# Kernel tuning notes

Measured on AMD Instinct MI355X. Metric: run time of the kernel, lower is better.

Reference implementation:

```python
import jax, jax.numpy as jnp
import numpy as np

N = 50000   # total nodes in batch
E = 640000  # directed edges
G = 64      # graphs in batch
D_IN = 128
D_H = 128
D_OUT = 10


def _glorot(key, shape):
    fan_in = shape[0]
    return jax.random.normal(key, shape, dtype=jnp.float32) / np.sqrt(fan_in)


def setup_inputs() -> dict:
    key = jax.random.key(0)
    ks = jax.random.split(key, 10)
    x = jax.random.normal(ks[0], (N, D_IN), dtype=jnp.float32)
    src = jax.random.randint(ks[1], (E,), 0, N, dtype=jnp.int32)
    dst = jax.random.randint(ks[2], (E,), 0, N, dtype=jnp.int32)
    batch = jnp.sort(jax.random.randint(ks[3], (N,), 0, G, dtype=jnp.int32))
    return {
        "x": x, "src": src, "dst": dst, "batch": batch,
        "W1": _glorot(ks[4], (D_IN, D_H)), "b1": jnp.zeros((D_H,), jnp.float32),
        "W2": _glorot(ks[5], (D_H, D_H)), "b2": jnp.zeros((D_H,), jnp.float32),
        "W3": _glorot(ks[6], (D_H, D_H)), "b3": jnp.zeros((D_H,), jnp.float32),
        "Wl": _glorot(ks[7], (D_H, D_OUT)), "bl": jnp.zeros((D_OUT,), jnp.float32),
    }


def gcn_conv(x, W, b, src, dst):
    """PyG GCNConv: add self-loops, symmetric deg^-1/2 normalization,
    linear transform, scatter-sum aggregation at dst, plus bias."""
    n = x.shape[0]
    loops = jnp.arange(n, dtype=src.dtype)
    s = jnp.concatenate([src, loops])  # [E+N]
    d = jnp.concatenate([dst, loops])
    deg = jax.ops.segment_sum(jnp.ones_like(d, dtype=x.dtype), d, num_segments=n)
    dinv = jnp.where(deg > 0, jax.lax.rsqrt(deg), 0.0)
    norm = dinv[s] * dinv[d]                        # [E+N]
    h = x @ W                                       # [N, D]
    out = jax.ops.segment_sum(h[s] * norm[:, None], d, num_segments=n)
    return out + b


def reference(x, src, dst, batch, W1, b1, W2, b2, W3, b3, Wl, bl):
    n = x.shape[0]
    h = jax.nn.relu(gcn_conv(x, W1, b1, src, dst))
    # dropout is a no-op in eval mode
    h = jax.nn.relu(gcn_conv(h, W2, b2, src, dst))
    h = gcn_conv(h, W3, b3, src, dst)
    # global_mean_pool over graph ids
    sums = jax.ops.segment_sum(h, batch, num_segments=G)            # [G, D]
    counts = jax.ops.segment_sum(jnp.ones((n,), h.dtype), batch, num_segments=G)
    pooled = sums / jnp.maximum(counts, 1.0)[:, None]
    logits = pooled @ Wl + bl                                       # [G, D_OUT]
    return jax.nn.log_softmax(logits, axis=1)
```

## Files before the change

### kernel.cpp

```cpp
#include <hip/hip_runtime.h>


constexpr int D = 128;
constexpr int DOUT = 10;
constexpr int PSPLIT = 8;
constexpr int BSH = 3;
constexpr int BCAP = 192;
constexpr int CPAD = 16;

using short8  = __attribute__((ext_vector_type(8))) short;
using float4v = __attribute__((ext_vector_type(4))) float;
using f32x2   = __attribute__((ext_vector_type(2))) float;

__device__ __forceinline__ ushort f2bf(float f) {
  uint u = __float_as_uint(f);
  return (ushort)((u + 0x7fffu + ((u >> 16) & 1u)) >> 16);
}
__device__ __forceinline__ float bf2f(ushort s) {
  return __uint_as_float(((uint)s) << 16);
}
__device__ __forceinline__ float bfhi(uint u) { return __uint_as_float(u & 0xffff0000u); }


__global__ void init_kernel(int* __restrict__ bcnt, int total) {
  int i = blockIdx.x * blockDim.x + threadIdx.x;
  if (i < total) bcnt[i] = 0;
}

__global__ void binfill_kernel(const int* __restrict__ src, const int* __restrict__ dst,
    int* __restrict__ bcnt, uint* __restrict__ buck, int e) {
  int i = blockIdx.x * blockDim.x + threadIdx.x;
  if (i >= e) return;
  int d = dst[i], s = src[i];
  int b = d >> BSH;
  int pos = atomicAdd(&bcnt[b * CPAD], 1);
  if (pos < BCAP)
    buck[(size_t)b * BCAP + pos] = (uint)s | ((uint)(d & ((1 << BSH) - 1)) << 16);
}

__global__ __launch_bounds__(256) void countb_kernel(const uint* __restrict__ buck,
    const int* __restrict__ bcnt, int* __restrict__ cnt, float* __restrict__ dinv,
    int* __restrict__ bsum, int n) {
  __shared__ int lc[256];
  const int base = blockIdx.x * 256;
  const int m = min(256, n - base);
  lc[threadIdx.x] = 0;
  __syncthreads();
  const int b0 = base >> BSH;
  #pragma unroll
  for (int bb = 0; bb < (256 >> BSH); ++bb) {
    int b = b0 + bb;
    if ((b << BSH) >= n) break;
    int c = min(bcnt[b * CPAD], BCAP);
    for (int i = threadIdx.x; i < c; i += 256)
      atomicAdd(&lc[(bb << BSH) + (int)(buck[(size_t)b * BCAP + i] >> 16)], 1);
  }
  __syncthreads();
  int v = lc[threadIdx.x];
  if ((int)threadIdx.x < m) {
    cnt[base + threadIdx.x] = v;
    dinv[base + threadIdx.x] = rsqrtf((float)(v + 1));
  }
  __shared__ int sd[256];
  sd[threadIdx.x] = ((int)threadIdx.x < m) ? v : 0;
  __syncthreads();
  for (int off = 128; off > 0; off >>= 1) {
    if (threadIdx.x < (unsigned)off) sd[threadIdx.x] += sd[threadIdx.x + off];
    __syncthreads();
  }
  if (threadIdx.x == 0) bsum[blockIdx.x] = sd[0];
}

__global__ __launch_bounds__(1024) void scan2_kernel(const int* __restrict__ bsum,
    int* __restrict__ boff, int nb, int* __restrict__ rowptr, int n) {
  __shared__ int sd[1024];
  int v = ((int)threadIdx.x < nb) ? bsum[threadIdx.x] : 0;
  sd[threadIdx.x] = v;
  __syncthreads();
  for (int off = 1; off < 1024; off <<= 1) {
    int t = (threadIdx.x >= (unsigned)off) ? sd[threadIdx.x - off] : 0;
    __syncthreads();
    sd[threadIdx.x] += t;
    __syncthreads();
  }
  if ((int)threadIdx.x < nb) boff[threadIdx.x] = sd[threadIdx.x] - v;
  if ((int)threadIdx.x == nb - 1) rowptr[n] = sd[threadIdx.x];
}

__global__ __launch_bounds__(256) void scatter_kernel(const uint* __restrict__ buck,
    const int* __restrict__ bcnt, const int* __restrict__ cnt,
    const int* __restrict__ boff, int* __restrict__ rowptr,
    const float* __restrict__ dinv, uint* __restrict__ epk, int n) {
  __shared__ int sd[256];
  __shared__ int lcur[256];
  const int base = blockIdx.x * 256;
  const int i = base + (int)threadIdx.x;
  int v = (i < n) ? cnt[i] : 0;
  sd[threadIdx.x] = v;
  __syncthreads();
  for (int off = 1; off < 256; off <<= 1) {
    int t = (threadIdx.x >= (unsigned)off) ? sd[threadIdx.x - off] : 0;
    __syncthreads();
    sd[threadIdx.x] += t;
    __syncthreads();
  }
  int rp = boff[blockIdx.x] + sd[threadIdx.x] - v;
  if (i < n) {
    rowptr[i] = rp;
    lcur[threadIdx.x] = rp;
  }
  __syncthreads();
  const int b0 = base >> BSH;
  #pragma unroll
  for (int bb = 0; bb < (256 >> BSH); ++bb) {
    int b = b0 + bb;
    if ((b << BSH) >= n) break;
    int c = min(bcnt[b * CPAD], BCAP);
    for (int j = threadIdx.x; j < c; j += 256) {
      uint rec = buck[(size_t)b * BCAP + j];
      int dl = (int)(rec >> 16);
      int s = (int)(rec & 0xffffu);
      int d = (b << BSH) + dl;
      int slot = atomicAdd(&lcur[(bb << BSH) + dl], 1);
      epk[slot] = (uint)s | ((uint)f2bf(dinv[s] * dinv[d]) << 16);
    }
  }
}

__global__ __launch_bounds__(256) void prepw_kernel(const float* __restrict__ W1,
    const float* __restrict__ W2, const float* __restrict__ W3, ushort* __restrict__ Wp) {
  const float* W = (blockIdx.y == 0) ? W1 : (blockIdx.y == 1) ? W2 : W3;
  ushort* Wpo = Wp + (size_t)blockIdx.y * 2048 * 8;
  int idx = blockIdx.x * 256 + threadIdx.x;
  int cf = idx >> 8, kk = (idx >> 6) & 3, lane = idx & 63;
  int k0 = kk * 32 + (lane >> 4) * 8;
  int c = cf * 16 + (lane & 15);
  uint p[4];
  #pragma unroll
  for (int h = 0; h < 4; ++h) {
    ushort lo = f2bf(W[(k0 + 2 * h) * D + c]);
    ushort hi = f2bf(W[(k0 + 2 * h + 1) * D + c]);
    p[h] = (uint)lo | ((uint)hi << 16);
  }
  uint4 w = make_uint4(p[0], p[1], p[2], p[3]);
  *(uint4*)(Wpo + idx * 8) = w;
}

__global__ __launch_bounds__(256) void gemm_mfma(const float* __restrict__ Ain,
    const ushort* __restrict__ Wp, uchar* __restrict__ out, int n) {
  __shared__ ushort wl[2048 * 8];
  const int tid = threadIdx.x;
  #pragma unroll
  for (int i = 0; i < 8; ++i) {
    int idx = tid + i * 256;
    *(uint4*)(&wl[idx * 8]) = *(const uint4*)(Wp + idx * 8);
  }
  __syncthreads();
  const int w = tid >> 6, lane = tid & 63;
  const int row0 = blockIdx.x * 64 + w * 16;
  int arow = row0 + (lane & 15);
  if (arow >= n) arow = n - 1;

  short8 a[4];
  const float* abase = Ain + (size_t)arow * D + ((lane >> 4) * 8);
  #pragma unroll
  for (int kk = 0; kk < 4; ++kk) {
    float4 f0 = *(const float4*)(abase + kk * 32);
    float4 f1 = *(const float4*)(abase + kk * 32 + 4);
    short8 v;
    v[0] = (short)f2bf(f0.x); v[1] = (short)f2bf(f0.y);
    v[2] = (short)f2bf(f0.z); v[3] = (short)f2bf(f0.w);
    v[4] = (short)f2bf(f1.x); v[5] = (short)f2bf(f1.y);
    v[6] = (short)f2bf(f1.z); v[7] = (short)f2bf(f1.w);
    a[kk] = v;
  }

  float4v acc[8] = {};
  #pragma unroll
  for (int kk = 0; kk < 4; ++kk) {
    #pragma unroll
    for (int cf = 0; cf < 8; ++cf) {
      short8 b = *(const short8*)(&wl[((cf * 4 + kk) * 64 + lane) * 8]);
      acc[cf] = __builtin_amdgcn_mfma_f32_16x16x32_bf16(a[kk], b, acc[cf], 0, 0, 0);
    }
  }
  const int crow = row0 + (lane >> 4) * 4;
  const int ccol = lane & 15;
  #pragma unroll
  for (int cf = 0; cf < 8; ++cf) {
    #pragma unroll
    for (int r = 0; r < 4; ++r) {
      if (crow + r < n) {
        int enc = __builtin_amdgcn_cvt_pk_fp8_f32(acc[cf][r], acc[cf][r], 0, false);
        out[(size_t)(crow + r) * D + cf * 16 + ccol] = (uchar)(enc & 0xff);
      }
    }
  }
}

__device__ __forceinline__ void agg_node(const uchar* __restrict__ h8,
    const int* __restrict__ rowptr, const uint* __restrict__ epk,
    const float* __restrict__ dinv, const float* __restrict__ bias,
    int node, int sub, int li, int relu,
    float& a0, float& a1, float& a2, float& a3) {
  const int beg = rowptr[node], end = rowptr[node + 1];
  a0 = a1 = a2 = a3 = 0.f;
  for (int e = beg; e < end; e += 16) {
    uint mm[8], rr[8];
    #pragma unroll
    for (int k = 0; k < 8; ++k)
      mm[k] = epk[min(e + 2 * k + sub, end - 1)];
    #pragma unroll
    for (int k = 0; k < 8; ++k)
      rr[k] = *(const uint*)(h8 + (size_t)(mm[k] & 0xffffu) * D + li * 4);
    #pragma unroll
    for (int k = 0; k < 8; ++k) {
      float wk = (e + 2 * k + sub < end) ? bfhi(mm[k]) : 0.f;
      f32x2 pa = __builtin_amdgcn_cvt_pk_f32_fp8(rr[k], false);
      f32x2 pb = __builtin_amdgcn_cvt_pk_f32_fp8(rr[k], true);
      a0 += pa[0] * wk;
      a1 += pa[1] * wk;
      a2 += pb[0] * wk;
      a3 += pb[1] * wk;
    }
  }
  a0 += __shfl_xor(a0, 32);
  a1 += __shfl_xor(a1, 32);
  a2 += __shfl_xor(a2, 32);
  a3 += __shfl_xor(a3, 32);
  const float di = dinv[node];
  const float dsq = di * di;
  uint sv = *(const uint*)(h8 + (size_t)node * D + li * 4);
  f32x2 sa = __builtin_amdgcn_cvt_pk_f32_fp8(sv, false);
  f32x2 sb = __builtin_amdgcn_cvt_pk_f32_fp8(sv, true);
  a0 += sa[0] * dsq;
  a1 += sa[1] * dsq;
  a2 += sb[0] * dsq;
  a3 += sb[1] * dsq;
  float4 bv = *(const float4*)(bias + li * 4);
  a0 += bv.x; a1 += bv.y; a2 += bv.z; a3 += bv.w;
  if (relu) {
    a0 = fmaxf(a0, 0.f); a1 = fmaxf(a1, 0.f);
    a2 = fmaxf(a2, 0.f); a3 = fmaxf(a3, 0.f);
  }
}

__global__ __launch_bounds__(256) void aggemm_kernel(const uchar* __restrict__ h8,
    const int* __restrict__ rowptr, const uint* __restrict__ epk,
    const float* __restrict__ dinv, const float* __restrict__ bias,
    const ushort* __restrict__ Wp, uchar* __restrict__ out8, int n) {
  __shared__ ushort At[16][136];
  const int wv = (int)(threadIdx.x >> 6);
  const int lane = (int)(threadIdx.x & 63);
  const int sub = lane >> 5;
  const int li = lane & 31;
  const int node0 = blockIdx.x * 16;
  #pragma unroll
  for (int t = 0; t < 4; ++t) {
    const int row = wv * 4 + t;
    const int node = node0 + row;
    if (node < n) {
      float a0, a1, a2, a3;
      agg_node(h8, rowptr, epk, dinv, bias, node, sub, li, 1, a0, a1, a2, a3);
      if (sub == 0) {
        uint2 pk;
        pk.x = (uint)f2bf(a0) | ((uint)f2bf(a1) << 16);
        pk.y = (uint)f2bf(a2) | ((uint)f2bf(a3) << 16);
        *(uint2*)(&At[row][li * 4]) = pk;
      }
    } else if (sub == 0) {
      *(uint2*)(&At[row][li * 4]) = make_uint2(0, 0);
    }
  }
  __syncthreads();
  const int r = lane & 15;
  const int koff = (lane >> 4) * 8;
  short8 a[4];
  #pragma unroll
  for (int kk = 0; kk < 4; ++kk)
    a[kk] = *(const short8*)(&At[r][koff + kk * 32]);
  const int crow = node0 + (lane >> 4) * 4;
  const int ccol = lane & 15;
  #pragma unroll
  for (int cc = 0; cc < 2; ++cc) {
    const int cf = wv * 2 + cc;
    float4v acc = {};
    #pragma unroll
    for (int kk = 0; kk < 4; ++kk) {
      short8 b = *(const short8*)(Wp + (size_t)((cf * 4 + kk) * 64 + lane) * 8);
      acc = __builtin_amdgcn_mfma_f32_16x16x32_bf16(a[kk], b, acc, 0, 0, 0);
    }
    #pragma unroll
    for (int r2 = 0; r2 < 4; ++r2) {
      if (crow + r2 < n) {
        int enc = __builtin_amdgcn_cvt_pk_fp8_f32(acc[r2], acc[r2], 0, false);
        out8[(size_t)(crow + r2) * D + cf * 16 + ccol] = (uchar)(enc & 0xff);
      }
    }
  }
}

__global__ __launch_bounds__(256) void agg_kernel(const uchar* __restrict__ h8,
    const int* __restrict__ rowptr, const uint* __restrict__ epk,
    const float* __restrict__ dinv, const float* __restrict__ bias,
    ushort* __restrict__ out, int n, int relu) {
  int node = (int)((blockIdx.x * blockDim.x + threadIdx.x) >> 6);
  if (node >= n) return;
  const int lane = threadIdx.x & 63;
  const int sub = lane >> 5;
  const int li = lane & 31;
  float a0, a1, a2, a3;
  agg_node(h8, rowptr, epk, dinv, bias, node, sub, li, relu, a0, a1, a2, a3);
  if (sub == 0) {
    uint2 pk;
    pk.x = (uint)f2bf(a0) | ((uint)f2bf(a1) << 16);
    pk.y = (uint)f2bf(a2) | ((uint)f2bf(a3) << 16);
    *(uint2*)(out + (size_t)node * D + li * 4) = pk;
  }
}

__global__ __launch_bounds__(256) void pool1_kernel(const ushort* __restrict__ act,
    const int* __restrict__ batch, float* __restrict__ pp, int n) {
  const int g = blockIdx.x;
  const int sp = blockIdx.y;
  int lo = 0, hi = n;
  while (lo < hi) { int mid = (lo + hi) >> 1; if (batch[mid] < g) lo = mid + 1; else hi = mid; }
  const int start = lo;
  hi = n;
  while (lo < hi) { int mid = (lo + hi) >> 1; if (batch[mid] <= g) lo = mid + 1; else hi = mid; }
  const int end = lo;
  const int len = end - start;
  const int per = (len + PSPLIT - 1) / PSPLIT;
  const int i0 = start + sp * per;
  const int i1 = min(i0 + per, end);

  const int rt = threadIdx.x >> 4;
  const int ds = threadIdx.x & 15;
  float acc[8] = {};
  for (int i = i0 + rt; i < i1; i += 16) {
    short8 v = *(const short8*)(act + (size_t)i * D + ds * 8);
    #pragma unroll
    for (int e2 = 0; e2 < 8; ++e2) acc[e2] += bf2f((ushort)v[e2]);
  }
  __shared__ float sd[256][8];
  #pragma unroll
  for (int e2 = 0; e2 < 8; ++e2) sd[threadIdx.x][e2] = acc[e2];
  __syncthreads();
  if (threadIdx.x < 128) {
    int d = threadIdx.x;
    int slice = d >> 3, e2 = d & 7;
    float s = 0.f;
    #pragma unroll
    for (int k = 0; k < 16; ++k) s += sd[k * 16 + slice][e2];
    pp[((size_t)g * PSPLIT + sp) * D + d] = s;
  }
}

__global__ __launch_bounds__(640) void head_kernel(const float* __restrict__ pp,
    const int* __restrict__ batch, const float* __restrict__ Wl,
    const float* __restrict__ bl, float* __restrict__ out, int n, int g) {
  __shared__ float pooled[64 * D];
  __shared__ float cnts[64];
  __shared__ float lg[64][DOUT];
  const int tid = threadIdx.x;
  if (tid < g) {
    int gg = tid;
    int lo = 0, hi = n;
    while (lo < hi) { int mid = (lo + hi) >> 1; if (batch[mid] < gg) lo = mid + 1; else hi = mid; }
    int start = lo;
    hi = n;
    while (lo < hi) { int mid = (lo + hi) >> 1; if (batch[mid] <= gg) lo = mid + 1; else hi = mid; }
    cnts[gg] = fmaxf((float)(lo - start), 1.f);
  }
  __syncthreads();
  for (int idx = tid; idx < g * D; idx += 640) {
    int gg = idx >> 7, d = idx & 127;
    float s = 0.f;
    #pragma unroll
    for (int sp = 0; sp < PSPLIT; ++sp) s += pp[((size_t)gg * PSPLIT + sp) * D + d];
    pooled[idx] = s / cnts[gg];
  }
  __syncthreads();
  int gi = tid / DOUT, o = tid % DOUT;
  if (gi < g) {
    float acc = bl[o];
    for (int d = 0; d < D; ++d) acc += pooled[gi * D + d] * Wl[d * DOUT + o];
    lg[gi][o] = acc;
  }
  __syncthreads();
  if (gi < g) {
    float m = -1e30f;
    for (int j = 0; j < DOUT; ++j) m = fmaxf(m, lg[gi][j]);
    float s = 0.f;
    for (int j = 0; j < DOUT; ++j) s += expf(lg[gi][j] - m);
    out[gi * DOUT + o] = lg[gi][o] - m - logf(s);
  }
}


extern "C" void kernel_launch(void* const* d_in, const int* in_sizes, int n_in,
                              void* d_out, int out_size, void* d_ws, size_t ws_size,
                              hipStream_t stream) {
  const float* x   = (const float*)d_in[0];
  const int* src   = (const int*)d_in[1];
  const int* dst   = (const int*)d_in[2];
  const int* batch = (const int*)d_in[3];
  const float* W1  = (const float*)d_in[4];
  const float* b1  = (const float*)d_in[5];
  const float* W2  = (const float*)d_in[6];
  const float* b2  = (const float*)d_in[7];
  const float* W3  = (const float*)d_in[8];
  const float* b3  = (const float*)d_in[9];
  const float* Wl  = (const float*)d_in[10];
  const float* bl  = (const float*)d_in[11];
  float* out = (float*)d_out;

  const int n = in_sizes[0] / D;
  const int e = in_sizes[1];
  const int g = out_size / DOUT;

  char* p = (char*)d_ws;
  auto alloc = [&](size_t bytes) {
    char* r = p;
    p += (bytes + 255) & ~(size_t)255;
    return r;
  };
  const int nb = (n + 255) / 256;
  const int NB = (n + (1 << BSH) - 1) >> BSH;
  int* cnt      = (int*)alloc((size_t)n * 4);
  int* rowptr   = (int*)alloc((size_t)(n + 1) * 4);
  float* dinv   = (float*)alloc((size_t)n * 4);
  int* bsum     = (int*)alloc((size_t)nb * 4);
  int* boff     = (int*)alloc((size_t)nb * 4);
  int* bcnt     = (int*)alloc((size_t)NB * CPAD * 4);
  uint* buck    = (uint*)alloc((size_t)NB * BCAP * 4);
  uint* epk     = (uint*)alloc((size_t)e * 4);
  ushort* Wp    = (ushort*)alloc(3 * 2048 * 16);
  ushort* bfB   = (ushort*)alloc((size_t)n * D * 2);
  uchar* tmpA   = (uchar*)alloc((size_t)n * D);
  uchar* tmpB   = (uchar*)alloc((size_t)n * D);
  float* pp     = (float*)alloc((size_t)g * PSPLIT * D * 4);
  (void)ws_size;

  const int B = 256;
  const int gridE = (e + B - 1) / B;

  init_kernel<<<(NB * CPAD + B - 1) / B, B, 0, stream>>>(bcnt, NB * CPAD);
  binfill_kernel<<<gridE, B, 0, stream>>>(src, dst, bcnt, buck, e);
  countb_kernel<<<nb, B, 0, stream>>>(buck, bcnt, cnt, dinv, bsum, n);
  scan2_kernel<<<1, 1024, 0, stream>>>(bsum, boff, nb, rowptr, n);
  scatter_kernel<<<nb, B, 0, stream>>>(buck, bcnt, cnt, boff, rowptr, dinv, epk, n);
  prepw_kernel<<<dim3(8, 3), B, 0, stream>>>(W1, W2, W3, Wp);

  const int gemmGrid = (n + 63) / 64;
  const int fuseGrid = (n + 15) / 16;
  const int aggGrid = (n * 64 + B - 1) / B;

  gemm_mfma<<<gemmGrid, B, 0, stream>>>(x, Wp, tmpA, n);
  aggemm_kernel<<<fuseGrid, B, 0, stream>>>(tmpA, rowptr, epk, dinv, b1,
                                            Wp + 2048 * 8, tmpB, n);
  aggemm_kernel<<<fuseGrid, B, 0, stream>>>(tmpB, rowptr, epk, dinv, b2,
                                            Wp + 2 * 2048 * 8, tmpA, n);
  agg_kernel<<<aggGrid, B, 0, stream>>>(tmpA, rowptr, epk, dinv, b3, bfB, n, 0);

  pool1_kernel<<<dim3(g, PSPLIT), B, 0, stream>>>(bfB, batch, pp, n);
  head_kernel<<<1, 640, 0, stream>>>(pp, batch, Wl, bl, out, n, g);
}
```

Baseline: 189.5 us.

## Fuse final GCN aggregation with mean-pool accumulation via shared and global atomics

Replaces the last aggregation kernel, which wrote a bf16 activation buffer, and the separate pooling kernel with one kernel. Each block aggregates 16 nodes and adds their results into per-graph shared-memory sums, then flushes them into split partial-pool slots with global atomics. The partial-pool buffer is now zeroed in the init kernel. This removes a full N×D intermediate write and re-read and one launch, at the cost of float atomics and a nondeterministic summation order.

```diff
diff --git a/kernel.cpp b/kernel.cpp
--- a/kernel.cpp
+++ b/kernel.cpp
@@ -22,9 +22,11 @@
 __device__ __forceinline__ float bfhi(uint u) { return __uint_as_float(u & 0xffff0000u); }
 
 
-__global__ void init_kernel(int* __restrict__ bcnt, int total) {
+__global__ void init_kernel(int* __restrict__ bcnt, int total,
+                            float* __restrict__ pp, int ppn) {
   int i = blockIdx.x * blockDim.x + threadIdx.x;
   if (i < total) bcnt[i] = 0;
+  if (i < ppn) pp[i] = 0.f;
 }
 
 __global__ void binfill_kernel(const int* __restrict__ src, const int* __restrict__ dst,
@@ -300,60 +302,52 @@
   }
 }
 
-__global__ __launch_bounds__(256) void agg_kernel(const uchar* __restrict__ h8,
+__global__ __launch_bounds__(256) void aggpool_kernel(const uchar* __restrict__ h8,
     const int* __restrict__ rowptr, const uint* __restrict__ epk,
     const float* __restrict__ dinv, const float* __restrict__ bias,
-    ushort* __restrict__ out, int n, int relu) {
-  int node = (int)((blockIdx.x * blockDim.x + threadIdx.x) >> 6);
-  if (node >= n) return;
-  const int lane = threadIdx.x & 63;
+    const int* __restrict__ batch, float* __restrict__ pp, int n) {
+  __shared__ float sums[2][D];
+  __shared__ int sg0;
+  const int wv = (int)(threadIdx.x >> 6);
+  const int lane = (int)(threadIdx.x & 63);
   const int sub = lane >> 5;
   const int li = lane & 31;
-  float a0, a1, a2, a3;
-  agg_node(h8, rowptr, epk, dinv, bias, node, sub, li, relu, a0, a1, a2, a3);
-  if (sub == 0) {
-    uint2 pk;
-    pk.x = (uint)f2bf(a0) | ((uint)f2bf(a1) << 16);
-    pk.y = (uint)f2bf(a2) | ((uint)f2bf(a3) << 16);
-    *(uint2*)(out + (size_t)node * D + li * 4) = pk;
-  }
-}
-
-__global__ __launch_bounds__(256) void pool1_kernel(const ushort* __restrict__ act,
-    const int* __restrict__ batch, float* __restrict__ pp, int n) {
-  const int g = blockIdx.x;
-  const int sp = blockIdx.y;
-  int lo = 0, hi = n;
-  while (lo < hi) { int mid = (lo + hi) >> 1; if (batch[mid] < g) lo = mid + 1; else hi = mid; }
-  const int start = lo;
-  hi = n;
-  while (lo < hi) { int mid = (lo + hi) >> 1; if (batch[mid] <= g) lo = mid + 1; else hi = mid; }
-  const int end = lo;
-  const int len = end - start;
-  const int per = (len + PSPLIT - 1) / PSPLIT;
-  const int i0 = start + sp * per;
-  const int i1 = min(i0 + per, end);
-
-  const int rt = threadIdx.x >> 4;
-  const int ds = threadIdx.x & 15;
-  float acc[8] = {};
-  for (int i = i0 + rt; i < i1; i += 16) {
-    short8 v = *(const short8*)(act + (size_t)i * D + ds * 8);
-    #pragma unroll
-    for (int e2 = 0; e2 < 8; ++e2) acc[e2] += bf2f((ushort)v[e2]);
-  }
-  __shared__ float sd[256][8];
-  #pragma unroll
-  for (int e2 = 0; e2 < 8; ++e2) sd[threadIdx.x][e2] = acc[e2];
-  __syncthreads();
-  if (threadIdx.x < 128) {
-    int d = threadIdx.x;
-    int slice = d >> 3, e2 = d & 7;
-    float s = 0.f;
-    #pragma unroll
-    for (int k = 0; k < 16; ++k) s += sd[k * 16 + slice][e2];
-    pp[((size_t)g * PSPLIT + sp) * D + d] = s;
-  }
+  const int node0 = blockIdx.x * 16;
+  for (int t = threadIdx.x; t < 2 * D; t += 256) ((float*)sums)[t] = 0.f;
+  if (threadIdx.x == 0) sg0 = batch[min(node0, n - 1)];
+  __syncthreads();
+  const int g0 = sg0;
+  const int sp = blockIdx.x & (PSPLIT - 1);
+  #pragma unroll
+  for (int t = 0; t < 4; ++t) {
+    const int node = node0 + wv * 4 + t;
+    if (node < n) {
+      float a0, a1, a2, a3;
+      agg_node(h8, rowptr, epk, dinv, bias, node, sub, li, 0, a0, a1, a2, a3);
+      if (sub == 0) {
+        const int gs = batch[node] - g0;
+        if (gs <= 1) {
+          atomicAdd(&sums[gs][li * 4 + 0], a0);
+          atomicAdd(&sums[gs][li * 4 + 1], a1);
+          atomicAdd(&sums[gs][li * 4 + 2], a2);
+          atomicAdd(&sums[gs][li * 4 + 3], a3);
+        } else {
+          float* dp = pp + ((size_t)batch[node] * PSPLIT + sp) * D + li * 4;
+          atomicAdd(&dp[0], a0);
+          atomicAdd(&dp[1], a1);
+          atomicAdd(&dp[2], a2);
+          atomicAdd(&dp[3], a3);
+        }
+      }
+    }
+  }
+  __syncthreads();
+  const int t = threadIdx.x;
+  const int gs = t >> 7, d = t & 127;
+  const int gg = g0 + gs;
+  float v = sums[gs][d];
+  if (v != 0.f)
+    atomicAdd(&pp[((size_t)gg * PSPLIT + sp) * D + d], v);
 }
 
 __global__ __launch_bounds__(640) void head_kernel(const float* __restrict__ pp,
@@ -427,6 +421,7 @@
   };
   const int nb = (n + 255) / 256;
   const int NB = (n + (1 << BSH) - 1) >> BSH;
+  const int ppn = g * PSPLIT * D;
   int* cnt      = (int*)alloc((size_t)n * 4);
   int* rowptr   = (int*)alloc((size_t)(n + 1) * 4);
   float* dinv   = (float*)alloc((size_t)n * 4);
@@ -436,16 +431,16 @@
   uint* buck    = (uint*)alloc((size_t)NB * BCAP * 4);
   uint* epk     = (uint*)alloc((size_t)e * 4);
   ushort* Wp    = (ushort*)alloc(3 * 2048 * 16);
-  ushort* bfB   = (ushort*)alloc((size_t)n * D * 2);
   uchar* tmpA   = (uchar*)alloc((size_t)n * D);
   uchar* tmpB   = (uchar*)alloc((size_t)n * D);
-  float* pp     = (float*)alloc((size_t)g * PSPLIT * D * 4);
+  float* pp     = (float*)alloc((size_t)ppn * 4);
   (void)ws_size;
 
   const int B = 256;
   const int gridE = (e + B - 1) / B;
-
-  init_kernel<<<(NB * CPAD + B - 1) / B, B, 0, stream>>>(bcnt, NB * CPAD);
+  const int initGrid = (NB * CPAD > ppn ? NB * CPAD : ppn);
+
+  init_kernel<<<(initGrid + B - 1) / B, B, 0, stream>>>(bcnt, NB * CPAD, pp, ppn);
   binfill_kernel<<<gridE, B, 0, stream>>>(src, dst, bcnt, buck, e);
   countb_kernel<<<nb, B, 0, stream>>>(buck, bcnt, cnt, dinv, bsum, n);
   scan2_kernel<<<1, 1024, 0, stream>>>(bsum, boff, nb, rowptr, n);
@@ -454,15 +449,13 @@
 
   const int gemmGrid = (n + 63) / 64;
   const int fuseGrid = (n + 15) / 16;
-  const int aggGrid = (n * 64 + B - 1) / B;
 
   gemm_mfma<<<gemmGrid, B, 0, stream>>>(x, Wp, tmpA, n);
   aggemm_kernel<<<fuseGrid, B, 0, stream>>>(tmpA, rowptr, epk, dinv, b1,
                                             Wp + 2048 * 8, tmpB, n);
   aggemm_kernel<<<fuseGrid, B, 0, stream>>>(tmpB, rowptr, epk, dinv, b2,
                                             Wp + 2 * 2048 * 8, tmpA, n);
-  agg_kernel<<<aggGrid, B, 0, stream>>>(tmpA, rowptr, epk, dinv, b3, bfB, n, 0);
-
-  pool1_kernel<<<dim3(g, PSPLIT), B, 0, stream>>>(bfB, batch, pp, n);
+  aggpool_kernel<<<fuseGrid, B, 0, stream>>>(tmpA, rowptr, epk, dinv, b3,
+                                             batch, pp, n);
   head_kernel<<<1, 640, 0, stream>>>(pp, batch, Wl, bl, out, n, g);
 }
```

Result: slower. 201.1 us (+6.1%).
